# Performance work log

Measured on AMD Instinct MI355X. Metric: run time of the kernel, lower is better.

Reference implementation:

```python
import jax, jax.numpy as jnp
import numpy as np

B, S, D, H = 4, 1024, 1024, 16
DK = D // H
NEG = -1e9


def setup_inputs() -> dict:
    key = jax.random.key(0)
    ks = jax.random.split(key, 14)
    sc = 1.0 / np.sqrt(D)
    inp = {
        "query": jax.random.normal(ks[0], (B, S, D), jnp.float32),
        "key": jax.random.normal(ks[1], (B, S, D), jnp.float32),
        "value": jax.random.normal(ks[2], (B, S, D), jnp.float32),
        "mask": jax.random.randint(ks[3], (B, S, S), 0, 2, jnp.int32),
        "group_prob": jax.random.uniform(ks[4], (B, S, S), jnp.float32),
        "Wq": jax.random.normal(ks[5], (D, D), jnp.float32) * sc,
        "bq": jnp.zeros((D,), jnp.float32),
        "Wk": jax.random.normal(ks[6], (D, D), jnp.float32) * sc,
        "bk": jnp.zeros((D,), jnp.float32),
        "Wv": jax.random.normal(ks[7], (D, D), jnp.float32) * sc,
        "bv": jnp.zeros((D,), jnp.float32),
        "Wo": jax.random.normal(ks[8], (D, D), jnp.float32) * sc,
        "bo": jnp.zeros((D,), jnp.float32),
    }
    return inp


def reference(query, key, value, mask, group_prob, Wq, bq, Wk, bk, Wv, bv, Wo, bo):
    # QKV projections, split heads: [B,S,D] -> [B,H,S,DK]
    def proj(x, W, b):
        return (x @ W.T + b).reshape(B, S, H, DK).transpose(0, 2, 1, 3)

    q = proj(query, Wq, bq)
    k = proj(key, Wk, bk)
    v = proj(value, Wv, bv)

    scores = jnp.einsum("bhqd,bhkd->bhqk", q, k) / jnp.sqrt(jnp.float32(DK))

    # group_prob branch: allowed where mask OR diagonal is nonzero
    diag = jnp.eye(S, dtype=jnp.int32)
    allowed = (mask[:, None, :, :] | diag[None, None, :, :]) != 0  # [B,1,S,S]
    scores = jnp.where(allowed, scores, NEG)

    p_attn = jax.nn.softmax(scores, axis=-1)
    p_attn = p_attn * group_prob[:, None, :, :]  # post-softmax group reweighting

    x = jnp.einsum("bhqk,bhkd->bhqd", p_attn, v)
    x = x.transpose(0, 2, 1, 3).reshape(B, S, D)
    return x @ Wo.T + bo
```

## Files before the change

kernel.cpp:

```cpp
#include <hip/hip_runtime.h>
#include <hip/hip_bf16.h>


#define AS1q __attribute__((address_space(1)))
#define AS3q __attribute__((address_space(3)))

typedef __attribute__((ext_vector_type(8))) __bf16 bf16x8;
typedef __attribute__((ext_vector_type(4))) float f32x4;
typedef __attribute__((ext_vector_type(8))) unsigned short u16x8;

#define GSTR 40

__device__ __forceinline__ void gload_lds16(const void* g, void* l) {
  __builtin_amdgcn_global_load_lds((const AS1q void*)g, (AS3q void*)l, 16, 0, 0);
}
__device__ __forceinline__ bf16x8 lds_read8(const unsigned short* p) {
  bf16x8 r;
  __builtin_memcpy(&r, __builtin_assume_aligned(p, 16), 16);
  return r;
}
__device__ __forceinline__ void lds_write8(unsigned short* p, const void* v) {
  __builtin_memcpy(__builtin_assume_aligned(p, 16), v, 16);
}
__device__ __forceinline__ u16x8 cvt8h(const float4 a, const float4 b) {
  const float fv[8] = {a.x, a.y, a.z, a.w, b.x, b.y, b.z, b.w};
  union { u16x8 v; __bf16 e[8]; } hh;
#pragma unroll
  for (int i = 0; i < 8; ++i) hh.e[i] = (__bf16)fv[i];
  return hh.v;
}
__device__ __forceinline__ void cvt8hl(const float4 a, const float4 b, u16x8* hi, u16x8* lo) {
  const float fv[8] = {a.x, a.y, a.z, a.w, b.x, b.y, b.z, b.w};
  union { u16x8 v; __bf16 e[8]; } hh, ll;
#pragma unroll
  for (int i = 0; i < 8; ++i) {
    const __bf16 h = (__bf16)fv[i];
    hh.e[i] = h;
    ll.e[i] = (__bf16)(fv[i] - (float)h);
  }
  *hi = hh.v; *lo = ll.v;
}
__device__ __forceinline__ unsigned short bfbits(float f) {
  const __bf16 h = (__bf16)f;
  unsigned short u; __builtin_memcpy(&u, &h, 2); return u;
}

__global__ __launch_bounds__(256) void k_gemm_qkv(
    const float* __restrict__ X0, const float* __restrict__ X1, const float* __restrict__ X2,
    const float* __restrict__ W0, const float* __restrict__ W1, const float* __restrict__ W2,
    const float* __restrict__ B0, const float* __restrict__ B1, const float* __restrict__ B2,
    unsigned short* __restrict__ O0, unsigned short* __restrict__ O1,
    unsigned short* __restrict__ O2)
{
  const int z = blockIdx.z;
  const float* X = (z == 0) ? X0 : (z == 1) ? X1 : X2;
  const float* W = (z == 0) ? W0 : (z == 1) ? W1 : W2;
  const float* Bi = (z == 0) ? B0 : (z == 1) ? B1 : B2;
  unsigned short* O = (z == 0) ? O0 : (z == 1) ? O1 : O2;

  const int bid = blockIdx.x;
  const int swz = (bid & 7) * 64 + (bid >> 3);
  const int n0 = (swz & 15) * 64, m0 = (swz >> 4) * 128;

  __shared__ alignas(16) unsigned short Ah[128 * GSTR];
  __shared__ alignas(16) unsigned short Bh[64 * GSTR];
  const int tid = threadIdx.x, l = tid & 63, w = tid >> 6;
  const int wr = w >> 1, wc = w & 1;

  f32x4 acc[4][2];
#pragma unroll
  for (int i = 0; i < 4; ++i)
#pragma unroll
    for (int j = 0; j < 2; ++j) acc[i][j] = (f32x4){0.f, 0.f, 0.f, 0.f};

  const int arow = tid >> 1, ac0 = (tid & 1) * 16;
  const int brow = tid >> 2, bc0 = (tid & 3) * 8;
  const float* xsrc = X + (size_t)(m0 + arow) * 1024 + ac0;
  const float* wsrc = W + (size_t)(n0 + brow) * 1024 + bc0;

  float4 fx[4], fw[2];
#pragma unroll
  for (int i = 0; i < 4; ++i) fx[i] = *(const float4*)(xsrc + i * 4);
#pragma unroll
  for (int i = 0; i < 2; ++i) fw[i] = *(const float4*)(wsrc + i * 4);

  for (int kt = 0; kt < 32; ++kt) {
    u16x8 xh[2], wh1;
    xh[0] = cvt8h(fx[0], fx[1]);
    xh[1] = cvt8h(fx[2], fx[3]);
    wh1 = cvt8h(fw[0], fw[1]);
    if (kt < 31) {
      const float* nx = xsrc + (kt + 1) * 32;
      const float* nw = wsrc + (kt + 1) * 32;
#pragma unroll
      for (int i = 0; i < 4; ++i) fx[i] = *(const float4*)(nx + i * 4);
#pragma unroll
      for (int i = 0; i < 2; ++i) fw[i] = *(const float4*)(nw + i * 4);
    }
    __syncthreads();
    lds_write8(&Ah[arow * GSTR + ac0], &xh[0]);
    lds_write8(&Ah[arow * GSTR + ac0 + 8], &xh[1]);
    lds_write8(&Bh[brow * GSTR + bc0], &wh1);
    __syncthreads();

    bf16x8 ah[4], bh[2];
#pragma unroll
    for (int mf = 0; mf < 4; ++mf) {
      const int r = wr * 64 + mf * 16 + (l & 15);
      ah[mf] = lds_read8(&Ah[r * GSTR + (l >> 4) * 8]);
    }
#pragma unroll
    for (int nf = 0; nf < 2; ++nf) {
      const int r = wc * 32 + nf * 16 + (l & 15);
      bh[nf] = lds_read8(&Bh[r * GSTR + (l >> 4) * 8]);
    }
#pragma unroll
    for (int mf = 0; mf < 4; ++mf)
#pragma unroll
      for (int nf = 0; nf < 2; ++nf)
        acc[mf][nf] = __builtin_amdgcn_mfma_f32_16x16x32_bf16(ah[mf], bh[nf], acc[mf][nf], 0, 0, 0);
  }

#pragma unroll
  for (int nf = 0; nf < 2; ++nf) {
    const int col = n0 + wc * 32 + nf * 16 + (l & 15);
    const float bias = Bi[col];
#pragma unroll
    for (int mf = 0; mf < 4; ++mf) {
      const int rbase = m0 + wr * 64 + mf * 16 + (l >> 4) * 4;
#pragma unroll
      for (int j = 0; j < 4; ++j)
        O[(size_t)(rbase + j) * 1024 + col] = bfbits(acc[mf][nf][j] + bias);
    }
  }
}

__global__ __launch_bounds__(256) void k_gemm_out(
    const unsigned short* __restrict__ X, const float* __restrict__ W,
    const float* __restrict__ Bi, float* __restrict__ Out)
{
  const int bid = blockIdx.x;
  const int swz = (bid & 7) * 128 + (bid >> 3);
  const int n0 = (swz & 15) * 64, m0 = (swz >> 4) * 64;

  __shared__ alignas(16) unsigned short Ah[64 * GSTR];
  __shared__ alignas(16) unsigned short Bh[64 * GSTR], Bl[64 * GSTR];
  const int tid = threadIdx.x, l = tid & 63, w = tid >> 6;
  const int wr = w >> 1, wc = w & 1;

  f32x4 acc[2][2];
#pragma unroll
  for (int i = 0; i < 2; ++i)
#pragma unroll
    for (int j = 0; j < 2; ++j) acc[i][j] = (f32x4){0.f, 0.f, 0.f, 0.f};

  const int srow = tid >> 2, sc0 = (tid & 3) * 8;
  const unsigned short* xsrc = X + (size_t)(m0 + srow) * 1024 + sc0;
  const float* wsrc = W + (size_t)(n0 + srow) * 1024 + sc0;

  u16x8 xcur = *(const u16x8*)xsrc;
  float4 fw[2];
#pragma unroll
  for (int i = 0; i < 2; ++i) fw[i] = *(const float4*)(wsrc + i * 4);

  for (int kt = 0; kt < 32; ++kt) {
    const u16x8 xstage = xcur;
    u16x8 wh1, wl1;
    cvt8hl(fw[0], fw[1], &wh1, &wl1);
    if (kt < 31) {
      xcur = *(const u16x8*)(xsrc + (kt + 1) * 32);
      const float* nw = wsrc + (kt + 1) * 32;
#pragma unroll
      for (int i = 0; i < 2; ++i) fw[i] = *(const float4*)(nw + i * 4);
    }
    __syncthreads();
    lds_write8(&Ah[srow * GSTR + sc0], &xstage);
    lds_write8(&Bh[srow * GSTR + sc0], &wh1);
    lds_write8(&Bl[srow * GSTR + sc0], &wl1);
    __syncthreads();

    bf16x8 ah[2], bh[2], bl[2];
#pragma unroll
    for (int mf = 0; mf < 2; ++mf) {
      const int r = wr * 32 + mf * 16 + (l & 15);
      ah[mf] = lds_read8(&Ah[r * GSTR + (l >> 4) * 8]);
    }
#pragma unroll
    for (int nf = 0; nf < 2; ++nf) {
      const int r = wc * 32 + nf * 16 + (l & 15);
      bh[nf] = lds_read8(&Bh[r * GSTR + (l >> 4) * 8]);
      bl[nf] = lds_read8(&Bl[r * GSTR + (l >> 4) * 8]);
    }
#pragma unroll
    for (int mf = 0; mf < 2; ++mf)
#pragma unroll
      for (int nf = 0; nf < 2; ++nf) {
        acc[mf][nf] = __builtin_amdgcn_mfma_f32_16x16x32_bf16(ah[mf], bh[nf], acc[mf][nf], 0, 0, 0);
        acc[mf][nf] = __builtin_amdgcn_mfma_f32_16x16x32_bf16(ah[mf], bl[nf], acc[mf][nf], 0, 0, 0);
      }
  }

#pragma unroll
  for (int nf = 0; nf < 2; ++nf) {
    const int col = n0 + wc * 32 + nf * 16 + (l & 15);
    const float bias = Bi[col];
#pragma unroll
    for (int mf = 0; mf < 2; ++mf) {
      const int rbase = m0 + wr * 32 + mf * 16 + (l >> 4) * 4;
#pragma unroll
      for (int j = 0; j < 4; ++j)
        Out[(size_t)(rbase + j) * 1024 + col] = acc[mf][nf][j] + bias;
    }
  }
}

__global__ __launch_bounds__(256) void k_attn(
    const unsigned short* Qh, const unsigned short* __restrict__ Kb,
    const unsigned short* __restrict__ Vb,
    const int* __restrict__ Mask, const float* __restrict__ Gp,
    unsigned short* Xo)
{
  const int h = blockIdx.x, qt = blockIdx.y, b = blockIdx.z;
  __shared__ alignas(16) unsigned short Kh[2][64 * 64];
  __shared__ alignas(16) unsigned short Vh[64 * 64];
  __shared__ alignas(16) unsigned short Ph[64 * 64];
  const int tid = threadIdx.x, l = tid & 63, w = tid >> 6;

  const unsigned short* kb_ = Kb + (size_t)b * 1048576 + h * 64;
  const unsigned short* vb_ = Vb + (size_t)b * 1048576 + h * 64;

  bf16x8 aq[2];
  {
    const int qrow = qt * 64 + w * 16 + (l & 15);
    const unsigned short* qp_ = Qh + ((size_t)(b * 1024 + qrow)) * 1024 + h * 64;
    aq[0] = lds_read8  (qp_ + (l >> 4) * 8);
    aq[1] = lds_read8(qp_ + 32 + (l >> 4) * 8);
  }

  f32x4 accO[4];
#pragma unroll
  for (int nf = 0; nf < 4; ++nf) accO[nf] = (f32x4){0.f, 0.f, 0.f, 0.f};
  float zacc[4] = {0.f, 0.f, 0.f, 0.f};

  const int qloc0 = w * 16 + (l >> 4) * 4;
  const int qg0 = qt * 64 + qloc0;
  const int mcol = l & 15;

  const int srcg8 = (((l & 7) ^ (l >> 3))) * 8;
  const int rowl = l >> 3;

  const int kb4 = (tid & 15) * 4, db4 = (tid >> 4) * 4;

  union U4 { unsigned int u[2]; unsigned short s[4]; };
  U4 vr[4];

#pragma unroll
  for (int I = 0; I < 2; ++I)
    gload_lds16(kb_ + (size_t)(I * 32 + w * 8 + rowl) * 1024 + srcg8,
                &Kh[0][I * 2048 + w * 512]);
#pragma unroll
  for (int i = 0; i < 4; ++i)
    __builtin_memcpy(&vr[i], vb_ + (size_t)(kb4 + i) * 1024 + db4, 8);

  int buf = 0;
  for (int kt = 0; kt < 16; ++kt) {
    __syncthreads();

#pragma unroll
    for (int i = 0; i < 4; ++i) {
      const int d = db4 + i;
      union { unsigned short s[4]; unsigned long long v; } pk;
#pragma unroll
      for (int u = 0; u < 4; ++u) pk.s[u] = vr[u].s[i];
      const int c = kb4 ^ ((d & 7) << 3);
      __builtin_memcpy(__builtin_assume_aligned(&Vh[d * 64 + c], 8), &pk.v, 8);
    }
    __syncthreads();

    if (kt < 15) {
#pragma unroll
      for (int I = 0; I < 2; ++I)
        gload_lds16(kb_ + (size_t)((kt + 1) * 64 + I * 32 + w * 8 + rowl) * 1024 + srcg8,
                    &Kh[buf ^ 1][I * 2048 + w * 512]);
#pragma unroll
      for (int i = 0; i < 4; ++i)
        __builtin_memcpy(&vr[i], vb_ + (size_t)((kt + 1) * 64 + kb4 + i) * 1024 + db4, 8);
    }

    int mk[4][4]; float gv[4][4];
#pragma unroll
    for (int j = 0; j < 4; ++j) {
      const size_t roff = ((size_t)(b * 1024 + qg0 + j)) << 10;
      const int* mr = Mask + roff + kt * 64 + mcol;
      const float* gr = Gp + roff + kt * 64 + mcol;
#pragma unroll
      for (int nf = 0; nf < 4; ++nf) { mk[nf][j] = mr[nf * 16]; gv[nf][j] = gr[nf * 16]; }
    }

#pragma unroll
    for (int nf = 0; nf < 4; ++nf) {
      f32x4 sacc = (f32x4){0.f, 0.f, 0.f, 0.f};
      const int kr = nf * 16 + (l & 15);
#pragma unroll
      for (int ks = 0; ks < 2; ++ks) {
        const int c = (ks * 32 + (l >> 4) * 8) ^ ((kr & 7) << 3);
        sacc = __builtin_amdgcn_mfma_f32_16x16x32_bf16(aq[ks], lds_read8(&Kh[buf][kr * 64 + c]), sacc, 0, 0, 0);
      }
      const int kg = kt * 64 + nf * 16 + mcol;
#pragma unroll
      for (int j = 0; j < 4; ++j) {
        const int qg = qg0 + j;
        const int allowed = mk[nf][j] | (qg == kg);
        const float e = allowed ? exp2f(fmaf(sacc[j], 0.18033688f, -17.31234049f)) : 0.f;
        zacc[j] += e;
        const int qloc = qloc0 + j;
        Ph[qloc * 64 + ((nf * 16 + mcol) ^ ((qloc & 7) << 3))] = bfbits(e * gv[nf][j]);
      }
    }
    bf16x8 pah[2];
    {
      const int ar = w * 16 + (l & 15);
#pragma unroll
      for (int ks = 0; ks < 2; ++ks) {
        const int c = (ks * 32 + (l >> 4) * 8) ^ ((ar & 7) << 3);
        pah[ks] = lds_read8(&Ph[ar * 64 + c]);
      }
    }
#pragma unroll
    for (int nf = 0; nf < 4; ++nf) {
      const int dr = nf * 16 + (l & 15);
#pragma unroll
      for (int ks = 0; ks < 2; ++ks) {
        const int c = (ks * 32 + (l >> 4) * 8) ^ ((dr & 7) << 3);
        accO[nf] = __builtin_amdgcn_mfma_f32_16x16x32_bf16(pah[ks], lds_read8(&Vh[dr * 64 + c]), accO[nf], 0, 0, 0);
      }
    }
    buf ^= 1;
  }

#pragma unroll
  for (int j = 0; j < 4; ++j) {
#pragma unroll
    for (int off = 1; off < 16; off <<= 1) zacc[j] += __shfl_xor(zacc[j], off, 64);
  }
  float rz[4];
#pragma unroll
  for (int j = 0; j < 4; ++j) rz[j] = 1.f / zacc[j];

#pragma unroll
  for (int nf = 0; nf < 4; ++nf) {
    const int d = nf * 16 + (l & 15);
#pragma unroll
    for (int j = 0; j < 4; ++j) {
      const int qg = qg0 + j;
      Xo[((size_t)(b * 1024 + qg)) * 1024 + h * 64 + d] = bfbits(accO[nf][j] * rz[j]);
    }
  }
}

extern "C" void kernel_launch(void* const* d_in, const int* in_sizes, int n_in,
                              void* d_out, int out_size, void* d_ws, size_t ws_size,
                              hipStream_t stream) {
  const float* query = (const float*)d_in[0];
  const float* key_in = (const float*)d_in[1];
  const float* value = (const float*)d_in[2];
  const int* mask = (const int*)d_in[3];
  const float* gp = (const float*)d_in[4];
  const float* Wq = (const float*)d_in[5];
  const float* bq = (const float*)d_in[6];
  const float* Wk = (const float*)d_in[7];
  const float* bk = (const float*)d_in[8];
  const float* Wv = (const float*)d_in[9];
  const float* bv = (const float*)d_in[10];
  const float* Wo = (const float*)d_in[11];
  const float* bo = (const float*)d_in[12];
  float* out = (float*)d_out;

  unsigned short* kp = (unsigned short*)d_ws;
  unsigned short* vp = kp + 4194304;
  unsigned short* qp = vp + 4194304;
  unsigned short* xo = qp;

  hipLaunchKernelGGL(k_gemm_qkv, dim3(512, 1, 3), dim3(256), 0, stream,
                     query, key_in, value, Wq, Wk, Wv, bq, bk, bv, qp, kp, vp);
  hipLaunchKernelGGL(k_attn, dim3(16, 16, 4), dim3(256), 0, stream,
                     qp, kp, vp, mask, gp, xo);
  hipLaunchKernelGGL(k_gemm_out, dim3(1024), dim3(256), 0, stream,
                     xo, Wo, bo, out);
}
```

Measured before the change: 182.1 us.

## Stage mask and group_prob tiles in LDS and remap blocks for L2 reuse

The attention kernel now loads each 64x64 mask and group_prob tile into shared memory with coalesced 16-byte global-to-LDS loads. Previously each lane did scattered 4-byte global reads. The grid is also flattened and remapped so that all 16 heads of a given (query tile, batch) pair share the same low index bits, which should place them on the same XCD. This lets the mask and probability rows, which every head re-reads, be reused from L2. The trade-off is 32KB of extra LDS per block, which lowers occupancy.

```diff
diff --git a/kernel.cpp b/kernel.cpp
--- a/kernel.cpp
+++ b/kernel.cpp
@@ -220,20 +220,28 @@
     const int* __restrict__ Mask, const float* __restrict__ Gp,
     unsigned short* Xo)
 {
-  const int h = blockIdx.x, qt = blockIdx.y, b = blockIdx.z;
+  const int i = blockIdx.x;
+  const int xc = i & 7, kk_ = i >> 3;
+  const int h = kk_ & 15, g = kk_ >> 4;
+  const int qb = g * 8 + xc;
+  const int qt = qb >> 2, b = qb & 3;
+
   __shared__ alignas(16) unsigned short Kh[2][64 * 64];
   __shared__ alignas(16) unsigned short Vh[64 * 64];
   __shared__ alignas(16) unsigned short Ph[64 * 64];
+  __shared__ alignas(16) int Ms[64 * 64];
+  __shared__ alignas(16) float Gs[64 * 64];
   const int tid = threadIdx.x, l = tid & 63, w = tid >> 6;
 
   const unsigned short* kb_ = Kb + (size_t)b * 1048576 + h * 64;
   const unsigned short* vb_ = Vb + (size_t)b * 1048576 + h * 64;
+  const int qrowbase = b * 1024 + qt * 64;
 
   bf16x8 aq[2];
   {
     const int qrow = qt * 64 + w * 16 + (l & 15);
     const unsigned short* qp_ = Qh + ((size_t)(b * 1024 + qrow)) * 1024 + h * 64;
-    aq[0] = lds_read8  (qp_ + (l >> 4) * 8);
+    aq[0] = lds_read8(qp_ + (l >> 4) * 8);
     aq[1] = lds_read8(qp_ + 32 + (l >> 4) * 8);
   }
 
@@ -246,11 +254,13 @@
   const int qg0 = qt * 64 + qloc0;
   const int mcol = l & 15;
 
-  const int srcg8 = (((l & 7) ^ (l >> 3))) * 8;
+  const int srcg8 = ((l & 7) ^ (l >> 3)) * 8;
   const int rowl = l >> 3;
 
+  const int* msrc = Mask + ((size_t)(qrowbase + w * 16 + (l >> 4)) << 10) + (l & 15) * 4;
+  const float* gsrc = Gp + ((size_t)(qrowbase + w * 16 + (l >> 4)) << 10) + (l & 15) * 4;
+
   const int kb4 = (tid & 15) * 4, db4 = (tid >> 4) * 4;
-
   union U4 { unsigned int u[2]; unsigned short s[4]; };
   U4 vr[4];
 
@@ -259,19 +269,24 @@
     gload_lds16(kb_ + (size_t)(I * 32 + w * 8 + rowl) * 1024 + srcg8,
                 &Kh[0][I * 2048 + w * 512]);
 #pragma unroll
-  for (int i = 0; i < 4; ++i)
-    __builtin_memcpy(&vr[i], vb_ + (size_t)(kb4 + i) * 1024 + db4, 8);
+  for (int ii = 0; ii < 4; ++ii)
+    __builtin_memcpy(&vr[ii], vb_ + (size_t)(kb4 + ii) * 1024 + db4, 8);
 
   int buf = 0;
   for (int kt = 0; kt < 16; ++kt) {
     __syncthreads();
 
 #pragma unroll
-    for (int i = 0; i < 4; ++i) {
-      const int d = db4 + i;
+    for (int I = 0; I < 4; ++I) {
+      gload_lds16(msrc + (size_t)kt * 64 + I * 4096, (char*)Ms + w * 4096 + I * 1024);
+      gload_lds16(gsrc + (size_t)kt * 64 + I * 4096, (char*)Gs + w * 4096 + I * 1024);
+    }
+#pragma unroll
+    for (int ii = 0; ii < 4; ++ii) {
+      const int d = db4 + ii;
       union { unsigned short s[4]; unsigned long long v; } pk;
 #pragma unroll
-      for (int u = 0; u < 4; ++u) pk.s[u] = vr[u].s[i];
+      for (int u = 0; u < 4; ++u) pk.s[u] = vr[u].s[ii];
       const int c = kb4 ^ ((d & 7) << 3);
       __builtin_memcpy(__builtin_assume_aligned(&Vh[d * 64 + c], 8), &pk.v, 8);
     }
@@ -283,18 +298,8 @@
         gload_lds16(kb_ + (size_t)((kt + 1) * 64 + I * 32 + w * 8 + rowl) * 1024 + srcg8,
                     &Kh[buf ^ 1][I * 2048 + w * 512]);
 #pragma unroll
-      for (int i = 0; i < 4; ++i)
-        __builtin_memcpy(&vr[i], vb_ + (size_t)((kt + 1) * 64 + kb4 + i) * 1024 + db4, 8);
-    }
-
-    int mk[4][4]; float gv[4][4];
-#pragma unroll
-    for (int j = 0; j < 4; ++j) {
-      const size_t roff = ((size_t)(b * 1024 + qg0 + j)) << 10;
-      const int* mr = Mask + roff + kt * 64 + mcol;
-      const float* gr = Gp + roff + kt * 64 + mcol;
-#pragma unroll
-      for (int nf = 0; nf < 4; ++nf) { mk[nf][j] = mr[nf * 16]; gv[nf][j] = gr[nf * 16]; }
+      for (int ii = 0; ii < 4; ++ii)
+        __builtin_memcpy(&vr[ii], vb_ + (size_t)((kt + 1) * 64 + kb4 + ii) * 1024 + db4, 8);
     }
 
 #pragma unroll
@@ -310,11 +315,13 @@
 #pragma unroll
       for (int j = 0; j < 4; ++j) {
         const int qg = qg0 + j;
-        const int allowed = mk[nf][j] | (qg == kg);
+        const int qloc = qloc0 + j;
+        const int mk = Ms[qloc * 64 + nf * 16 + mcol];
+        const float gvv = Gs[qloc * 64 + nf * 16 + mcol];
+        const int allowed = mk | (qg == kg);
         const float e = allowed ? exp2f(fmaf(sacc[j], 0.18033688f, -17.31234049f)) : 0.f;
         zacc[j] += e;
-        const int qloc = qloc0 + j;
-        Ph[qloc * 64 + ((nf * 16 + mcol) ^ ((qloc & 7) << 3))] = bfbits(e * gv[nf][j]);
+        Ph[qloc * 64 + ((nf * 16 + mcol) ^ ((qloc & 7) << 3))] = bfbits(e * gvv);
       }
     }
     bf16x8 pah[2];
@@ -383,7 +390,7 @@
 
   hipLaunchKernelGGL(k_gemm_qkv, dim3(512, 1, 3), dim3(256), 0, stream,
                      query, key_in, value, Wq, Wk, Wv, bq, bk, bv, qp, kp, vp);
-  hipLaunchKernelGGL(k_attn, dim3(16, 16, 4), dim3(256), 0, stream,
+  hipLaunchKernelGGL(k_attn, dim3(1024), dim3(256), 0, stream,
                      qp, kp, vp, mask, gp, xo);
   hipLaunchKernelGGL(k_gemm_out, dim3(1024), dim3(256), 0, stream,
                      xo, Wo, bo, out);
```

New measurement: 186.5 us. 2.4% more time.
